# Performance work log

Hardware: AMD Instinct MI355X
Metric: run time of the kernel (lower is better)

## Reference

```python
import jax, jax.numpy as jnp
import numpy as np

DIM = 1024
NUM_HEADS = 16
HEAD_DIM = DIM // NUM_HEADS
SCALE = HEAD_DIM ** -0.5


def setup_inputs() -> dict:
    key = jax.random.key(0)
    ks = jax.random.split(key, 11)
    B, N, M = 8, 1024, 1024
    s = DIM ** -0.5  # init scale for weights
    return {
        "x": jax.random.normal(ks[0], (B, N, DIM), jnp.float32),
        "context": jax.random.normal(ks[1], (B, M, DIM), jnp.float32),
        "Wq": jax.random.normal(ks[2], (DIM, DIM), jnp.float32) * s,
        "bq": jax.random.normal(ks[3], (DIM,), jnp.float32) * 0.01,
        "Wk": jax.random.normal(ks[4], (DIM, DIM), jnp.float32) * s,
        "bk": jax.random.normal(ks[5], (DIM,), jnp.float32) * 0.01,
        "Wv": jax.random.normal(ks[6], (DIM, DIM), jnp.float32) * s,
        "bv": jax.random.normal(ks[7], (DIM,), jnp.float32) * 0.01,
        "Wo": jax.random.normal(ks[8], (DIM, DIM), jnp.float32) * s,
        "bo": jax.random.normal(ks[9], (DIM,), jnp.float32) * 0.01,
    }


def reference(x, context, Wq, bq, Wk, bk, Wv, bv, Wo, bo):
    B, N, _ = x.shape
    M = context.shape[1]
    # Linear projections (torch Linear: x @ W.T + b; here W stored as [in, out])
    q = x @ Wq + bq            # [B, N, DIM]
    k = context @ Wk + bk      # [B, M, DIM]
    v = context @ Wv + bv      # [B, M, DIM]
    # split heads: b n (h d) -> b h n d
    q = q.reshape(B, N, NUM_HEADS, HEAD_DIM).transpose(0, 2, 1, 3)
    k = k.reshape(B, M, NUM_HEADS, HEAD_DIM).transpose(0, 2, 1, 3)
    v = v.reshape(B, M, NUM_HEADS, HEAD_DIM).transpose(0, 2, 1, 3)
    dots = jnp.einsum('bhnd,bhmd->bhnm', q, k) * SCALE
    attn = jax.nn.softmax(dots, axis=-1)
    out = jnp.einsum('bhnm,bhmd->bhnd', attn, v)   # [B, H, N, d]
    out = out.transpose(0, 2, 1, 3).reshape(B, N, DIM)  # b h n d -> b n (h d)
    return out @ Wo + bo
```

## Files before the change

### kernel.cpp

```cpp
#include <hip/hip_runtime.h>

typedef unsigned short u16;
typedef __attribute__((ext_vector_type(8))) short bf16x8;
typedef __attribute__((ext_vector_type(4))) float f32x4;
typedef __attribute__((ext_vector_type(16))) float f32x16;
typedef __attribute__((ext_vector_type(4))) unsigned u32x4;

#define MFMA16 __builtin_amdgcn_mfma_f32_16x16x32_bf16
#define MFMA32 __builtin_amdgcn_mfma_f32_32x32x16_bf16

__device__ __forceinline__ u16 f2b(float f) {
  unsigned u = __builtin_bit_cast(unsigned, f);
  u = (u + 0x7fffu + ((u >> 16) & 1u)) >> 16;
  return (u16)u;
}

__device__ __forceinline__ void gload_lds16(const u16* g, u16* l) {
  __builtin_amdgcn_global_load_lds((const __attribute__((address_space(1))) void*)g,
                                   (__attribute__((address_space(3))) void*)l, 16, 0, 0);
}

__global__ void prep(const float* __restrict__ x, const float* __restrict__ ctx,
                     u16* __restrict__ xb, u16* __restrict__ cb,
                     const float* __restrict__ w0, const float* __restrict__ w1,
                     const float* __restrict__ w2, const float* __restrict__ w3,
                     u16* __restrict__ o0, u16* __restrict__ o1,
                     u16* __restrict__ o2, u16* __restrict__ o3) {
  __shared__ float t[64][65];
  const int z = blockIdx.z;
  const int tid = threadIdx.x;
  if (z < 2) {
    int i = blockIdx.x * blockDim.x + tid;
    const float* in = z ? ctx : x;
    u16* out = z ? cb : xb;
    float4 v = reinterpret_cast<const float4*>(in)[i];
    reinterpret_cast<ushort4*>(out)[i] = make_ushort4(f2b(v.x), f2b(v.y), f2b(v.z), f2b(v.w));
    return;
  }
  const int id = blockIdx.x;
  if (id >= 1024) return;
  const int wsel = id >> 8;
  const float* src = wsel == 0 ? w0 : wsel == 1 ? w1 : wsel == 2 ? w2 : w3;
  u16* dst = wsel == 0 ? o0 : wsel == 1 ? o1 : wsel == 2 ? o2 : o3;
  const int r0 = ((id >> 4) & 15) * 64, c0 = (id & 15) * 64;
  #pragma unroll
  for (int it = 0; it < 4; ++it) {
    int row = it * 16 + (tid >> 4);
    int col = (tid & 15) * 4;
    float4 v = *reinterpret_cast<const float4*>(&src[(size_t)(r0 + row) * 1024 + c0 + col]);
    t[row][col] = v.x; t[row][col + 1] = v.y; t[row][col + 2] = v.z; t[row][col + 3] = v.w;
  }
  __syncthreads();
  #pragma unroll
  for (int it = 0; it < 2; ++it) {
    int c = it * 32 + (tid >> 3);
    int r8 = (tid & 7) * 8;
    u16 tmp[8];
    #pragma unroll
    for (int k = 0; k < 8; ++k) tmp[k] = f2b(t[r8 + k][c]);
    uint4 pk;
    pk.x = (unsigned)tmp[0] | ((unsigned)tmp[1] << 16);
    pk.y = (unsigned)tmp[2] | ((unsigned)tmp[3] << 16);
    pk.z = (unsigned)tmp[4] | ((unsigned)tmp[5] << 16);
    pk.w = (unsigned)tmp[6] | ((unsigned)tmp[7] << 16);
    *reinterpret_cast<uint4*>(&dst[(size_t)(c0 + c) * 1024 + r0 + r8]) = pk;
  }
}

__device__ __forceinline__ void gemm_core(const u16* __restrict__ A, const u16* __restrict__ Wt,
                                          f32x4 (&acc)[4][4], int brow, int bcol,
                                          u16* __restrict__ smem) {
  const int tid = threadIdx.x;
  const int lane = tid & 63;
  const int w = tid >> 6;
  const int wr = w >> 1, wc = w & 1;
  const int l16 = lane & 15, g = lane >> 4;

  auto stage = [&](int buf, int kt) {
    #pragma unroll
    for (int it = 0; it < 4; ++it) {
      int c = it * 256 + tid;
      int row = (c >> 2) & 127;
      int ks = c >> 9;
      int k8 = c & 3;
      const size_t gofs = (size_t)kt * 64 + ks * 32 + k8 * 8;
      gload_lds16(&A[(size_t)(brow + row) * 1024 + gofs],
                  &smem[buf * 8192 + (it * 256 + w * 64) * 8]);
      gload_lds16(&Wt[(size_t)(bcol + row) * 1024 + gofs],
                  &smem[16384 + buf * 8192 + (it * 256 + w * 64) * 8]);
    }
  };

  stage(0, 0);
  __syncthreads();
  int cur = 0;
  for (int kt = 0; kt < 16; ++kt) {
    if (kt < 15) stage(cur ^ 1, kt + 1);
    const u16* As = &smem[cur * 8192];
    const u16* Bs = &smem[16384 + cur * 8192];
    #pragma unroll
    for (int ks = 0; ks < 2; ++ks) {
      bf16x8 a[4], b[4];
      const int kb = ks * 4096 + g * 8;
      #pragma unroll
      for (int mi = 0; mi < 4; ++mi)
        a[mi] = *reinterpret_cast<const bf16x8*>(&As[kb + (wr * 64 + mi * 16 + l16) * 32]);
      #pragma unroll
      for (int ni = 0; ni < 4; ++ni)
        b[ni] = *reinterpret_cast<const bf16x8*>(&Bs[kb + (wc * 64 + ni * 16 + l16) * 32]);
      #pragma unroll
      for (int mi = 0; mi < 4; ++mi)
        #pragma unroll
        for (int ni = 0; ni < 4; ++ni)
          acc[mi][ni] = MFMA16(a[mi], b[ni], acc[mi][ni], 0, 0, 0);
    }
    __syncthreads();
    cur ^= 1;
  }
}

__global__ __launch_bounds__(256, 2) void gemm_qkv(const u16* __restrict__ xb, const u16* __restrict__ cb,
                                                   const u16* __restrict__ Wqt, const u16* __restrict__ Wkt,
                                                   const u16* __restrict__ Wvt,
                                                   const float* __restrict__ bq, const float* __restrict__ bk,
                                                   const float* __restrict__ bv,
                                                   u16* __restrict__ Qb, u16* __restrict__ Kf,
                                                   u16* __restrict__ Vf) {
  __shared__ u16 smem[32768];
  const int z = blockIdx.z;
  const u16* A = z == 0 ? xb : cb;
  const u16* W = z == 0 ? Wqt : z == 1 ? Wkt : Wvt;
  const float* bias = z == 0 ? bq : z == 1 ? bk : bv;
  const int brow = blockIdx.x * 128, bcol = blockIdx.y * 128;
  f32x4 acc[4][4] = {};
  gemm_core(A, W, acc, brow, bcol, smem);

  const int lane = threadIdx.x & 63;
  const int w = threadIdx.x >> 6;
  const int wr = w >> 1, wc = w & 1;
  const int l16 = lane & 15, g = lane >> 4;
  const float CS = 0.125f * 1.44269504089f;
  u16* T = &smem[w * 5120];

  if (z < 2) {
    #pragma unroll
    for (int ni = 0; ni < 4; ++ni) {
      const float bz = bias[bcol + wc * 64 + ni * 16 + l16];
      #pragma unroll
      for (int mi = 0; mi < 4; ++mi) {
        f32x4 v = acc[mi][ni];
        #pragma unroll
        for (int j = 0; j < 4; ++j) {
          float val = v[j] + bz;
          if (z == 0) val *= CS;
          T[(mi * 16 + g * 4 + j) * 80 + ni * 16 + l16] = f2b(val);
        }
      }
    }
    const int r0b = brow + wr * 64;
    const int colb = bcol + wc * 64;
    if (z == 0) {
      #pragma unroll
      for (int it = 0; it < 8; ++it) {
        const int rl = it * 8 + (lane >> 3);
        const int c8 = (lane & 7) * 8;
        bf16x8 val = *reinterpret_cast<const bf16x8*>(&T[rl * 80 + c8]);
        *reinterpret_cast<bf16x8*>(&Qb[(size_t)(r0b + rl) * 1024 + colb + c8]) = val;
      }
    } else {
      const int h = colb >> 6;
      const int bb = r0b >> 10;
      const int kt = (r0b & 1023) >> 6;
      u16* kb2 = &Kf[(((size_t)(bb * 16 + h)) * 16 + kt) * 4096];
      #pragma unroll
      for (int it = 0; it < 8; ++it) {
        const int rl = it * 8 + (lane >> 3);
        const int c8 = (lane & 7) * 8;
        bf16x8 val = *reinterpret_cast<const bf16x8*>(&T[rl * 80 + c8]);
        const int chunk = (c8 >> 4) * 128 + (rl >> 5) * 64 + ((c8 >> 3) & 1) * 32 + (rl & 31);
        *reinterpret_cast<bf16x8*>(&kb2[chunk * 8]) = val;
      }
    }
  } else {
    #pragma unroll
    for (int ni = 0; ni < 4; ++ni) {
      const float bz = bias[bcol + wc * 64 + ni * 16 + l16];
      #pragma unroll
      for (int mi = 0; mi < 4; ++mi) {
        f32x4 v = acc[mi][ni];
        #pragma unroll
        for (int j = 0; j < 4; ++j)
          T[(ni * 16 + l16) * 80 + mi * 16 + g * 4 + j] = f2b(v[j] + bz);
      }
    }
    const int h = (bcol + wc * 64) >> 6;
    const int m0 = brow + wr * 64;
    const int bb = m0 >> 10;
    const int kt = (m0 & 1023) >> 6;
    u16* vb = &Vf[(((size_t)(bb * 16 + h)) * 16 + kt) * 4096];
    #pragma unroll
    for (int it = 0; it < 8; ++it) {
      const int d = it * 8 + (lane >> 3);
      const int m8 = (lane & 7) * 8;
      bf16x8 val = *reinterpret_cast<const bf16x8*>(&T[d * 80 + m8]);
      const int chunk = (m8 >> 4) * 128 + (d >> 5) * 64 + ((m8 >> 3) & 1) * 32 + (d & 31);
      *reinterpret_cast<bf16x8*>(&vb[chunk * 8]) = val;
    }
  }
}

__global__ __launch_bounds__(256, 2) void gemm_o(const u16* __restrict__ A, const u16* __restrict__ Wt,
                                                 const float* __restrict__ bias, float* __restrict__ outp) {
  __shared__ u16 smem[32768];
  const int brow = blockIdx.x * 128, bcol = blockIdx.y * 128;
  f32x4 acc[4][4] = {};
  gemm_core(A, Wt, acc, brow, bcol, smem);
  const int lane = threadIdx.x & 63;
  const int w = threadIdx.x >> 6;
  const int wr = w >> 1, wc = w & 1;
  const int l16 = lane & 15, g = lane >> 4;
  #pragma unroll
  for (int ni = 0; ni < 4; ++ni) {
    const int col = bcol + wc * 64 + ni * 16 + l16;
    const float bz = bias[col];
    #pragma unroll
    for (int mi = 0; mi < 4; ++mi) {
      const int r0 = brow + wr * 64 + mi * 16 + g * 4;
      f32x4 v = acc[mi][ni];
      #pragma unroll
      for (int j = 0; j < 4; ++j) outp[(size_t)(r0 + j) * 1024 + col] = v[j] + bz;
    }
  }
}

__global__ __launch_bounds__(256, 2) void attn2(const u16* __restrict__ Q, const u16* __restrict__ Kf,
                                                const u16* __restrict__ Vf, u16* __restrict__ AO) {
  __shared__ u16 Ks[2][64 * 64];
  __shared__ u16 Vs[2][64 * 64];
  const int tid = threadIdx.x, lane = tid & 63, w = tid >> 6;
  const int l32 = lane & 31, u = lane >> 5;
  const int id = blockIdx.x;
  const int v = (id & 7) * 128 + (id >> 3);
  const int qt = v & 7, h = (v >> 3) & 15, b = v >> 7;
  const int q0 = qt * 128 + w * 32;

  bf16x8 qf[4];
  {
    const u16* qp = &Q[(size_t)(b * 1024 + q0 + l32) * 1024 + h * 64 + u * 8];
    #pragma unroll
    for (int m = 0; m < 4; ++m) qf[m] = *reinterpret_cast<const bf16x8*>(qp + m * 16);
  }

  f32x16 o0 = {}, o1 = {};
  float lr = 0.f;

  const u16* Kbh = Kf + (size_t)(b * 16 + h) * 65536;
  const u16* Vbh = Vf + (size_t)(b * 16 + h) * 65536;

  auto stage = [&](int buf, int kt) {
    #pragma unroll
    for (int it = 0; it < 2; ++it) {
      const int c = (it * 256 + tid) * 8;
      gload_lds16(&Kbh[kt * 4096 + c], &Ks[buf][(it * 256 + w * 64) * 8]);
      gload_lds16(&Vbh[kt * 4096 + c], &Vs[buf][(it * 256 + w * 64) * 8]);
    }
  };

  stage(0, 0);
  __syncthreads();
  int cur = 0;

  for (int kt = 0; kt < 16; ++kt) {
    if (kt < 15) stage(cur ^ 1, kt + 1);

    f32x16 s0 = {}, s1 = {};
    __builtin_amdgcn_s_setprio(1);
    #pragma unroll
    for (int m = 0; m < 4; ++m) {
      bf16x8 k0 = *reinterpret_cast<const bf16x8*>(&Ks[cur][m * 1024 + lane * 8]);
      bf16x8 k1 = *reinterpret_cast<const bf16x8*>(&Ks[cur][m * 1024 + 512 + lane * 8]);
      s0 = MFMA32(k0, qf[m], s0, 0, 0, 0);
      s1 = MFMA32(k1, qf[m], s1, 0, 0, 0);
    }
    __builtin_amdgcn_s_setprio(0);

    unsigned W0[8], W1[8];
    #pragma unroll
    for (int j = 0; j < 8; ++j) {
      const int r = 4 * (j >> 1) + 2 * (j & 1);
      float pa0 = __builtin_amdgcn_exp2f(s0[r]);
      float pb0 = __builtin_amdgcn_exp2f(s0[r + 1]);
      float pa1 = __builtin_amdgcn_exp2f(s1[r]);
      float pb1 = __builtin_amdgcn_exp2f(s1[r + 1]);
      lr += (pa0 + pb0) + (pa1 + pb1);
      asm("v_cvt_pk_bf16_f32 %0, %1, %2" : "=v"(W0[j]) : "v"(pa0), "v"(pb0));
      asm("v_cvt_pk_bf16_f32 %0, %1, %2" : "=v"(W1[j]) : "v"(pa1), "v"(pb1));
    }

    unsigned paw[4][4];
    #pragma unroll
    for (int ks = 0; ks < 4; ++ks) {
      const int ksl = ks & 1;
      #pragma unroll
      for (int p = 0; p < 2; ++p) {
        unsigned x = (ks < 2) ? W0[4 * ksl + p] : W1[4 * ksl + p];
        unsigned y = (ks < 2) ? W0[4 * ksl + 2 + p] : W1[4 * ksl + 2 + p];
        asm("v_permlane32_swap_b32 %0, %1" : "+v"(x), "+v"(y));
        paw[ks][p] = x;
        paw[ks][2 + p] = y;
      }
    }

    __builtin_amdgcn_s_setprio(1);
    #pragma unroll
    for (int ks = 0; ks < 4; ++ks) {
      bf16x8 pa = __builtin_bit_cast(bf16x8, u32x4{paw[ks][0], paw[ks][1], paw[ks][2], paw[ks][3]});
      bf16x8 v0 = *reinterpret_cast<const bf16x8*>(&Vs[cur][ks * 1024 + lane * 8]);
      bf16x8 v1 = *reinterpret_cast<const bf16x8*>(&Vs[cur][ks * 1024 + 512 + lane * 8]);
      o0 = MFMA32(pa, v0, o0, 0, 0, 0);
      o1 = MFMA32(pa, v1, o1, 0, 0, 0);
    }
    __builtin_amdgcn_s_setprio(0);

    __syncthreads();
    cur ^= 1;
  }

  float sum = lr + __shfl_xor(lr, 32);
  float rinv = 1.0f / sum;
  u16* aop = &AO[(size_t)(b * 1024 + q0) * 1024 + h * 64 + l32];
  #pragma unroll
  for (int r = 0; r < 16; ++r) {
    const int ql = (r & 3) + 8 * (r >> 2) + 4 * u;
    int ri_i = __builtin_amdgcn_ds_bpermute((ql + (u << 5)) << 2, __builtin_bit_cast(int, rinv));
    float ri = __builtin_bit_cast(float, ri_i);
    aop[(size_t)ql * 1024] = f2b(o0[r] * ri);
    aop[(size_t)ql * 1024 + 32] = f2b(o1[r] * ri);
  }
}

extern "C" void kernel_launch(void* const* d_in, const int* in_sizes, int n_in,
                              void* d_out, int out_size, void* d_ws, size_t ws_size,
                              hipStream_t stream) {
  const float* x   = (const float*)d_in[0];
  const float* ctx = (const float*)d_in[1];
  const float* Wq  = (const float*)d_in[2];
  const float* bq  = (const float*)d_in[3];
  const float* Wk  = (const float*)d_in[4];
  const float* bk  = (const float*)d_in[5];
  const float* Wv  = (const float*)d_in[6];
  const float* bv  = (const float*)d_in[7];
  const float* Wo  = (const float*)d_in[8];
  const float* bo  = (const float*)d_in[9];
  float* out = (float*)d_out;
  char* ws = (char*)d_ws;

  u16* xb  = (u16*)(ws + (size_t)0);
  u16* cb  = (u16*)(ws + ((size_t)16 << 20));
  u16* Qb  = (u16*)(ws + ((size_t)32 << 20));
  u16* Kf  = (u16*)(ws + ((size_t)48 << 20));
  u16* Vf  = (u16*)(ws + ((size_t)64 << 20));
  u16* Wqt = (u16*)(ws + ((size_t)80 << 20));
  u16* Wkt = (u16*)(ws + ((size_t)82 << 20));
  u16* Wvt = (u16*)(ws + ((size_t)84 << 20));
  u16* Wot = (u16*)(ws + ((size_t)86 << 20));

  prep<<<dim3(8192, 1, 3), 256, 0, stream>>>(x, ctx, xb, cb, Wq, Wk, Wv, Wo, Wqt, Wkt, Wvt, Wot);
  gemm_qkv<<<dim3(64, 8, 3), 256, 0, stream>>>(xb, cb, Wqt, Wkt, Wvt, bq, bk, bv, Qb, Kf, Vf);
  attn2<<<dim3(1024), 256, 0, stream>>>(Qb, Kf, Vf, xb );
  gemm_o<<<dim3(64, 8), 256, 0, stream>>>(xb, Wot, bo, out);
}
```

Measured before the change: 152.3 us.

## Replace QKV GEMM with 256x256-tile, 8-wave, double-buffered direct-to-LDS kernel

```diff
diff --git a/kernel.cpp b/kernel.cpp
--- a/kernel.cpp
+++ b/kernel.cpp
@@ -67,6 +67,148 @@
   }
 }
 
+__global__ __launch_bounds__(512, 2) void gemm_qkv256(
+    const u16* __restrict__ xb, const u16* __restrict__ cb,
+    const u16* __restrict__ Wqt, const u16* __restrict__ Wkt, const u16* __restrict__ Wvt,
+    const float* __restrict__ bq, const float* __restrict__ bk, const float* __restrict__ bv,
+    u16* __restrict__ Qb, u16* __restrict__ Kf, u16* __restrict__ Vf) {
+  __shared__ u16 smem[65536];
+  const int tid = threadIdx.x;
+  const int lane = tid & 63;
+  const int w = tid >> 6;
+  const int wr = w >> 2, wc = w & 3;
+  const int l16 = lane & 15, g = (lane >> 4) & 3;
+  const int z = blockIdx.z;
+  const u16* Ain = z == 0 ? xb : cb;
+  const u16* W = z == 0 ? Wqt : z == 1 ? Wkt : Wvt;
+  const float* bias = z == 0 ? bq : z == 1 ? bk : bv;
+  const int brow = blockIdx.x * 256, bcol = blockIdx.y * 256;
+
+  int aoff[4], boff[4];
+  #pragma unroll
+  for (int it = 0; it < 4; ++it) {
+    const int c = it * 512 + tid;
+    const int kk = ((c >> 6) & 1) * 32 + ((c >> 4) & 3) * 8;
+    const int arow = (c >> 10) * 128 + ((c >> 7) & 7) * 16 + (c & 15);
+    aoff[it] = (brow + arow) * 1024 + kk;
+    const int bcolc = (c >> 9) * 64 + ((c >> 7) & 3) * 16 + (c & 15);
+    boff[it] = (bcol + bcolc) * 1024 + kk;
+  }
+  auto stage = [&](int buf, int t) {
+    u16* db = smem + buf * 32768;
+    #pragma unroll
+    for (int it = 0; it < 4; ++it)
+      gload_lds16(&Ain[(size_t)(aoff[it] + t * 64)], db + (it * 512 + w * 64) * 8);
+    #pragma unroll
+    for (int it = 0; it < 4; ++it)
+      gload_lds16(&W[(size_t)(boff[it] + t * 64)], db + 16384 + (it * 512 + w * 64) * 8);
+  };
+
+  f32x4 acc[8][4] = {};
+  stage(0, 0);
+  stage(1, 1);
+  asm volatile("s_waitcnt vmcnt(8)" ::: "memory");
+  __builtin_amdgcn_sched_barrier(0);
+  __builtin_amdgcn_s_barrier();
+  __builtin_amdgcn_sched_barrier(0);
+
+  for (int t = 0; t < 16; ++t) {
+    const int cur = t & 1;
+    const u16* As = smem + cur * 32768;
+    const u16* Bs = As + 16384;
+    bf16x8 bfr[2][4];
+    #pragma unroll
+    for (int ks = 0; ks < 2; ++ks)
+      #pragma unroll
+      for (int ni = 0; ni < 4; ++ni)
+        bfr[ks][ni] = *reinterpret_cast<const bf16x8*>(&Bs[(wc * 512 + ni * 128 + ks * 64 + lane) * 8]);
+    __builtin_amdgcn_s_setprio(1);
+    #pragma unroll
+    for (int mi = 0; mi < 8; ++mi) {
+      bf16x8 a0 = *reinterpret_cast<const bf16x8*>(&As[(wr * 1024 + mi * 128 + lane) * 8]);
+      bf16x8 a1 = *reinterpret_cast<const bf16x8*>(&As[(wr * 1024 + mi * 128 + 64 + lane) * 8]);
+      #pragma unroll
+      for (int ni = 0; ni < 4; ++ni)
+        acc[mi][ni] = MFMA16(a1, bfr[1][ni], MFMA16(a0, bfr[0][ni], acc[mi][ni], 0, 0, 0), 0, 0, 0);
+    }
+    __builtin_amdgcn_s_setprio(0);
+    __builtin_amdgcn_sched_barrier(0);
+    __builtin_amdgcn_s_barrier();
+    __builtin_amdgcn_sched_barrier(0);
+    if (t < 14) {
+      stage(cur, t + 2);
+      asm volatile("s_waitcnt vmcnt(8)" ::: "memory");
+    } else {
+      asm volatile("s_waitcnt vmcnt(0)" ::: "memory");
+    }
+    __builtin_amdgcn_sched_barrier(0);
+    __builtin_amdgcn_s_barrier();
+    __builtin_amdgcn_sched_barrier(0);
+  }
+
+  u16* T = smem + w * 4608;
+  float bz[4];
+  #pragma unroll
+  for (int ni = 0; ni < 4; ++ni) bz[ni] = bias[bcol + wc * 64 + ni * 16 + l16];
+  const float CS = 0.125f * 1.44269504089f;
+  const int h = (bcol + wc * 64) >> 6;
+  #pragma unroll
+  for (int p = 0; p < 2; ++p) {
+    if (z < 2) {
+      #pragma unroll
+      for (int mi4 = 0; mi4 < 4; ++mi4)
+        #pragma unroll
+        for (int ni = 0; ni < 4; ++ni) {
+          f32x4 v = acc[p * 4 + mi4][ni];
+          #pragma unroll
+          for (int j = 0; j < 4; ++j) {
+            float val = v[j] + bz[ni];
+            if (z == 0) val *= CS;
+            T[(mi4 * 16 + g * 4 + j) * 72 + ni * 16 + l16] = f2b(val);
+          }
+        }
+      if (z == 0) {
+        #pragma unroll
+        for (int it = 0; it < 8; ++it) {
+          const int rl = it * 8 + (lane >> 3), c8 = (lane & 7) * 8;
+          bf16x8 val = *reinterpret_cast<const bf16x8*>(&T[rl * 72 + c8]);
+          *reinterpret_cast<bf16x8*>(
+              &Qb[(size_t)(brow + wr * 128 + p * 64 + rl) * 1024 + bcol + wc * 64 + c8]) = val;
+        }
+      } else {
+        #pragma unroll
+        for (int it = 0; it < 8; ++it) {
+          const int rl = it * 8 + (lane >> 3), c8 = (lane & 7) * 8;
+          bf16x8 val = *reinterpret_cast<const bf16x8*>(&T[rl * 72 + c8]);
+          const int m = brow + wr * 128 + p * 64 + rl;
+          const int bb = m >> 10, kt = (m & 1023) >> 6;
+          const int chunk = (c8 >> 4) * 128 + ((m & 63) >> 5) * 64 + ((c8 >> 3) & 1) * 32 + (m & 31);
+          *reinterpret_cast<bf16x8*>(&Kf[(((size_t)(bb * 16 + h)) * 16 + kt) * 4096 + chunk * 8]) = val;
+        }
+      }
+    } else {
+      #pragma unroll
+      for (int mi4 = 0; mi4 < 4; ++mi4)
+        #pragma unroll
+        for (int ni = 0; ni < 4; ++ni) {
+          f32x4 v = acc[p * 4 + mi4][ni];
+          #pragma unroll
+          for (int j = 0; j < 4; ++j)
+            T[(ni * 16 + l16) * 72 + mi4 * 16 + g * 4 + j] = f2b(v[j] + bz[ni]);
+        }
+      #pragma unroll
+      for (int it = 0; it < 8; ++it) {
+        const int d = it * 8 + (lane >> 3), m8 = (lane & 7) * 8;
+        bf16x8 val = *reinterpret_cast<const bf16x8*>(&T[d * 72 + m8]);
+        const int m = brow + wr * 128 + p * 64 + m8;
+        const int bb = m >> 10, kt = (m & 1023) >> 6;
+        const int chunk = (m8 >> 4) * 128 + (d >> 5) * 64 + ((m8 >> 3) & 1) * 32 + (d & 31);
+        *reinterpret_cast<bf16x8*>(&Vf[(((size_t)(bb * 16 + h)) * 16 + kt) * 4096 + chunk * 8]) = val;
+      }
+    }
+  }
+}
+
 __device__ __forceinline__ void gemm_core(const u16* __restrict__ A, const u16* __restrict__ Wt,
                                           f32x4 (&acc)[4][4], int brow, int bcol,
                                           u16* __restrict__ smem) {
@@ -116,96 +258,6 @@
     }
     __syncthreads();
     cur ^= 1;
-  }
-}
-
-__global__ __launch_bounds__(256, 2) void gemm_qkv(const u16* __restrict__ xb, const u16* __restrict__ cb,
-                                                   const u16* __restrict__ Wqt, const u16* __restrict__ Wkt,
-                                                   const u16* __restrict__ Wvt,
-                                                   const float* __restrict__ bq, const float* __restrict__ bk,
-                                                   const float* __restrict__ bv,
-                                                   u16* __restrict__ Qb, u16* __restrict__ Kf,
-                                                   u16* __restrict__ Vf) {
-  __shared__ u16 smem[32768];
-  const int z = blockIdx.z;
-  const u16* A = z == 0 ? xb : cb;
-  const u16* W = z == 0 ? Wqt : z == 1 ? Wkt : Wvt;
-  const float* bias = z == 0 ? bq : z == 1 ? bk : bv;
-  const int brow = blockIdx.x * 128, bcol = blockIdx.y * 128;
-  f32x4 acc[4][4] = {};
-  gemm_core(A, W, acc, brow, bcol, smem);
-
-  const int lane = threadIdx.x & 63;
-  const int w = threadIdx.x >> 6;
-  const int wr = w >> 1, wc = w & 1;
-  const int l16 = lane & 15, g = lane >> 4;
-  const float CS = 0.125f * 1.44269504089f;
-  u16* T = &smem[w * 5120];
-
-  if (z < 2) {
-    #pragma unroll
-    for (int ni = 0; ni < 4; ++ni) {
-      const float bz = bias[bcol + wc * 64 + ni * 16 + l16];
-      #pragma unroll
-      for (int mi = 0; mi < 4; ++mi) {
-        f32x4 v = acc[mi][ni];
-        #pragma unroll
-        for (int j = 0; j < 4; ++j) {
-          float val = v[j] + bz;
-          if (z == 0) val *= CS;
-          T[(mi * 16 + g * 4 + j) * 80 + ni * 16 + l16] = f2b(val);
-        }
-      }
-    }
-    const int r0b = brow + wr * 64;
-    const int colb = bcol + wc * 64;
-    if (z == 0) {
-      #pragma unroll
-      for (int it = 0; it < 8; ++it) {
-        const int rl = it * 8 + (lane >> 3);
-        const int c8 = (lane & 7) * 8;
-        bf16x8 val = *reinterpret_cast<const bf16x8*>(&T[rl * 80 + c8]);
-        *reinterpret_cast<bf16x8*>(&Qb[(size_t)(r0b + rl) * 1024 + colb + c8]) = val;
-      }
-    } else {
-      const int h = colb >> 6;
-      const int bb = r0b >> 10;
-      const int kt = (r0b & 1023) >> 6;
-      u16* kb2 = &Kf[(((size_t)(bb * 16 + h)) * 16 + kt) * 4096];
-      #pragma unroll
-      for (int it = 0; it < 8; ++it) {
-        const int rl = it * 8 + (lane >> 3);
-        const int c8 = (lane & 7) * 8;
-        bf16x8 val = *reinterpret_cast<const bf16x8*>(&T[rl * 80 + c8]);
-        const int chunk = (c8 >> 4) * 128 + (rl >> 5) * 64 + ((c8 >> 3) & 1) * 32 + (rl & 31);
-        *reinterpret_cast<bf16x8*>(&kb2[chunk * 8]) = val;
-      }
-    }
-  } else {
-    #pragma unroll
-    for (int ni = 0; ni < 4; ++ni) {
-      const float bz = bias[bcol + wc * 64 + ni * 16 + l16];
-      #pragma unroll
-      for (int mi = 0; mi < 4; ++mi) {
-        f32x4 v = acc[mi][ni];
-        #pragma unroll
-        for (int j = 0; j < 4; ++j)
-          T[(ni * 16 + l16) * 80 + mi * 16 + g * 4 + j] = f2b(v[j] + bz);
-      }
-    }
-    const int h = (bcol + wc * 64) >> 6;
-    const int m0 = brow + wr * 64;
-    const int bb = m0 >> 10;
-    const int kt = (m0 & 1023) >> 6;
-    u16* vb = &Vf[(((size_t)(bb * 16 + h)) * 16 + kt) * 4096];
-    #pragma unroll
-    for (int it = 0; it < 8; ++it) {
-      const int d = it * 8 + (lane >> 3);
-      const int m8 = (lane & 7) * 8;
-      bf16x8 val = *reinterpret_cast<const bf16x8*>(&T[d * 80 + m8]);
-      const int chunk = (m8 >> 4) * 128 + (d >> 5) * 64 + ((m8 >> 3) & 1) * 32 + (d & 31);
-      *reinterpret_cast<bf16x8*>(&vb[chunk * 8]) = val;
-    }
   }
 }
 
@@ -366,7 +418,7 @@
   u16* Wot = (u16*)(ws + ((size_t)86 << 20));
 
   prep<<<dim3(8192, 1, 3), 256, 0, stream>>>(x, ctx, xb, cb, Wq, Wk, Wv, Wo, Wqt, Wkt, Wvt, Wot);
-  gemm_qkv<<<dim3(64, 8, 3), 256, 0, stream>>>(xb, cb, Wqt, Wkt, Wvt, bq, bk, bv, Qb, Kf, Vf);
+  gemm_qkv256<<<dim3(32, 4, 3), 512, 0, stream>>>(xb, cb, Wqt, Wkt, Wvt, bq, bk, bv, Qb, Kf, Vf);
   attn2<<<dim3(1024), 256, 0, stream>>>(Qb, Kf, Vf, xb );
   gemm_o<<<dim3(64, 8), 256, 0, stream>>>(xb, Wot, bo, out);
 }
```

Result: slower. 172.5 us (+13.3%).
